# Optimization experiments

Measured on AMD Instinct MI355X. Metric: run time of the kernel, lower is better.

## Reference

```python
import jax, jax.numpy as jnp
import numpy as np

N = 50000   # nodes
E = 600000  # directed edges (self-loops added inside reference, per GCNConv default)
G = 64      # graphs in the batch
D = 128     # in_features
H = 128     # hidden_channels
C = 10      # num_classes


def setup_inputs() -> dict:
    key = jax.random.key(0)
    ks = jax.random.split(key, 9)
    x = jax.random.normal(ks[0], (N, D), dtype=jnp.float32)
    edge_index = jax.random.randint(ks[1], (2, E), 0, N, dtype=jnp.int64)
    batch = jnp.sort(jax.random.randint(ks[2], (N,), 0, G, dtype=jnp.int64))
    # GCNConv weights (glorot-ish scale) and biases; final linear layer
    W1 = jax.random.normal(ks[3], (D, H), dtype=jnp.float32) / np.sqrt(D).astype(np.float32)
    b1 = jnp.zeros((H,), dtype=jnp.float32)
    W2 = jax.random.normal(ks[4], (H, H), dtype=jnp.float32) / np.sqrt(H).astype(np.float32)
    b2 = jnp.zeros((H,), dtype=jnp.float32)
    Wlin = jax.random.normal(ks[5], (H, C), dtype=jnp.float32) / np.sqrt(H).astype(np.float32)
    blin = jnp.zeros((C,), dtype=jnp.float32)
    return {"x": x, "W1": W1, "b1": b1, "W2": W2, "b2": b2,
            "Wlin": Wlin, "blin": blin, "edge_index": edge_index, "batch": batch}


def _gcn_conv(x, W, b, row, col, norm):
    # x' = D^{-1/2}(A+I)D^{-1/2} (x W) + b ; aggregate messages from row (src) into col (dst)
    h = x @ W                                   # [N, H] dense GEMM
    msg = norm[:, None] * h[row]                # gather by source index [E+N, H]
    out = jax.ops.segment_sum(msg, col, num_segments=N)  # scatter-add to targets
    return out + b


def reference(x, W1, b1, W2, b2, Wlin, blin, edge_index, batch):
    loops = jnp.arange(N, dtype=edge_index.dtype)
    row = jnp.concatenate([edge_index[0], loops])   # sources (+ self loops)
    col = jnp.concatenate([edge_index[1], loops])   # targets (+ self loops)
    # symmetric degree normalization (degrees >= 1 thanks to self loops)
    deg = jax.ops.segment_sum(jnp.ones_like(col, dtype=jnp.float32), col, num_segments=N)
    dinv = jax.lax.rsqrt(deg)
    norm = dinv[row] * dinv[col]                    # [E+N]

    h = jax.nn.relu(_gcn_conv(x, W1, b1, row, col, norm))
    h = _gcn_conv(h, W2, b2, row, col, norm)

    # global mean pool over graphs
    sums = jax.ops.segment_sum(h, batch, num_segments=G)                       # [G, H]
    cnt = jax.ops.segment_sum(jnp.ones((N,), dtype=jnp.float32), batch, num_segments=G)
    pooled = sums / jnp.maximum(cnt, 1.0)[:, None]

    return pooled @ Wlin + blin                     # logits [G, C]
```

## Files before the change

### kernel.cpp

```cpp
#include <hip/hip_runtime.h>

#define NN 50000
#define NE 600000
#define NG 64
#define DIM 128
#define NCLS 10
#define SB 196
#define NNP 50176
#define KBLK 392
#define KCH 128
#define CAP 64
#define E2B ((NE / 2 + 255) / 256)
#define BSW_TAIL_START ((size_t)(NN >> 5) * 4096)

typedef unsigned short ushort;
typedef unsigned char uchar;
typedef __attribute__((ext_vector_type(8))) short short8;
typedef __attribute__((ext_vector_type(4))) float float4v;
typedef __attribute__((ext_vector_type(2))) float float2v;

__device__ __forceinline__ ushort f2bf(float f) {
    unsigned u = __float_as_uint(f);
    u += 0x7fff + ((u >> 16) & 1);
    return (ushort)(u >> 16);
}
__device__ __forceinline__ uchar f2fp8(float f) {
    int p = __builtin_amdgcn_cvt_pk_fp8_f32(f, f, 0, false);
    return (uchar)(p & 0xff);
}
__device__ __forceinline__ void accfp8(float* a, uint2 v) {
    float2v p0 = __builtin_amdgcn_cvt_pk_f32_fp8(v.x, false);
    float2v p1 = __builtin_amdgcn_cvt_pk_f32_fp8(v.x, true);
    float2v p2 = __builtin_amdgcn_cvt_pk_f32_fp8(v.y, false);
    float2v p3 = __builtin_amdgcn_cvt_pk_f32_fp8(v.y, true);
    a[0] += p0[0]; a[1] += p0[1]; a[2] += p1[0]; a[3] += p1[1];
    a[4] += p2[0]; a[5] += p2[1]; a[6] += p3[0]; a[7] += p3[1];
}
__device__ __forceinline__ uint2 ldrow(const uchar* __restrict__ Hs, int r, size_t off) {
    return *(const uint2*)(Hs + (size_t)r * DIM + off);
}

__global__ void k_init(int* __restrict__ cnt, const float* __restrict__ W1,
                       ushort* __restrict__ Wsw, float* __restrict__ T,
                       ushort* __restrict__ Bsw) {
    int b = blockIdx.x, t = threadIdx.x;
    if (b < SB) {
        int i = b * 256 + t;
        if (i < NN) cnt[i] = 0;
    } else if (b < SB + 64) {
        int tid = (b - SB) * 256 + t;
        int j = tid & 7;
        int lane = (tid >> 3) & 63;
        int frag = tid >> 9;
        int nt = frag >> 2, kc = frag & 3;
        int k = kc * 32 + (lane >> 4) * 8 + j;
        int n = nt * 16 + (lane & 15);
        Wsw[tid] = f2bf(W1[k * DIM + n]);
    } else if (b < SB + 64 + 784) {
        float4* w4 = (float4*)T;
        int base = (b - SB - 64) * 256 + t;
#pragma unroll
        for (int i = 0; i < 4; ++i)
            w4[base + i * 200704] = make_float4(0.f, 0.f, 0.f, 0.f);
    } else {
        int idx = (b - (SB + 64 + 784)) * 256 + t;
        ((float4*)(Bsw + BSW_TAIL_START))[idx] = make_float4(0.f, 0.f, 0.f, 0.f);
    }
}

__global__ void k_fill(const int* __restrict__ row, const int* __restrict__ col,
                       int* __restrict__ cnt, ushort* __restrict__ ell) {
    int e = (blockIdx.x * blockDim.x + threadIdx.x) * 2;
    if (e < NE) {
        int2 r = *(const int2*)(row + e);
        int2 c = *(const int2*)(col + e);
        int p0 = atomicAdd(&cnt[c.x], 1);
        if (p0 < CAP) ell[(size_t)c.x * CAP + p0] = (ushort)r.x;
        int p1 = atomicAdd(&cnt[c.y], 1);
        if (p1 < CAP) ell[(size_t)c.y * CAP + p1] = (ushort)r.y;
    }
}

__global__ __launch_bounds__(256) void k_gemm_mfma(const float* __restrict__ Ain,
                                                   const ushort* __restrict__ Wsw,
                                                   const int* __restrict__ cnt,
                                                   uchar* __restrict__ Hs) {
    const int t = threadIdx.x;
    const int wave = t >> 6, lane = t & 63;
    const int m = lane & 15, quad = lane >> 4;
    const int row0 = blockIdx.x * 64 + wave * 16;

    short8 bfrag[8][4];
#pragma unroll
    for (int nt = 0; nt < 8; ++nt)
#pragma unroll
        for (int kc = 0; kc < 4; ++kc)
            bfrag[nt][kc] = *(const short8*)(Wsw + ((nt * 4 + kc) * 64 + lane) * 8);

    float4v acc[8];
#pragma unroll
    for (int nt = 0; nt < 8; ++nt) acc[nt] = (float4v){0.f, 0.f, 0.f, 0.f};

    const int row = row0 + m;
    const int rclamp = row < NN ? row : NN - 1;

#pragma unroll
    for (int kc = 0; kc < 4; ++kc) {
        const float* ap = Ain + (size_t)rclamp * DIM + kc * 32 + quad * 8;
        float4 v0 = *(const float4*)ap;
        float4 v1 = *(const float4*)(ap + 4);
        union { short8 v; ushort u[8]; } tmp;
        tmp.u[0] = f2bf(v0.x); tmp.u[1] = f2bf(v0.y);
        tmp.u[2] = f2bf(v0.z); tmp.u[3] = f2bf(v0.w);
        tmp.u[4] = f2bf(v1.x); tmp.u[5] = f2bf(v1.y);
        tmp.u[6] = f2bf(v1.z); tmp.u[7] = f2bf(v1.w);
        short8 a = tmp.v;
#pragma unroll
        for (int nt = 0; nt < 8; ++nt)
            acc[nt] = __builtin_amdgcn_mfma_f32_16x16x32_bf16(a, bfrag[nt][kc], acc[nt], 0, 0, 0);
    }

#pragma unroll
    for (int reg = 0; reg < 4; ++reg) {
        int r = row0 + quad * 4 + reg;
        if (r < NN) {
            float d = rsqrtf(1.0f + (float)cnt[r]);
#pragma unroll
            for (int nt = 0; nt < 8; ++nt)
                Hs[(size_t)r * DIM + nt * 16 + m] = f2fp8(d * acc[nt][reg]);
        }
    }
}

__global__ __launch_bounds__(256) void k_gather_ell(const ushort* __restrict__ ell,
                                                    const int* __restrict__ deg,
                                                    const int* __restrict__ batch,
                                                    const float* __restrict__ bias,
                                                    const uchar* __restrict__ Hs,
                                                    float* __restrict__ T,
                                                    ushort* __restrict__ Bsw) {
    const int t = threadIdx.x, b = blockIdx.x;
    const int tn = t >> 4, lane = t & 15;
    const int node = b * 16 + tn;
    const ushort* rowp = ell + (size_t)node * CAP;
    int end = min(deg[node], CAP);
    const float d = rsqrtf(1.0f + (float)deg[node]);
    float* Trow = T + (size_t)batch[node] * NNP;
    const size_t off = (size_t)lane * 8;

    float a[8] = {0.f, 0.f, 0.f, 0.f, 0.f, 0.f, 0.f, 0.f};
    accfp8(a, ldrow(Hs, node, off));
    if (lane == 0) atomicAdd(&Trow[node], d);

    int e = 0;
    for (; e + 8 <= end; e += 8) {
        uint4 iv = *(const uint4*)(rowp + e);
        int r0 = iv.x & 0xffff, r1 = iv.x >> 16;
        int r2 = iv.y & 0xffff, r3 = iv.y >> 16;
        int r4 = iv.z & 0xffff, r5 = iv.z >> 16;
        int r6 = iv.w & 0xffff, r7 = iv.w >> 16;
        if (lane < 8) atomicAdd(&Trow[rowp[e + lane]], d);
        uint2 v0 = ldrow(Hs, r0, off), v1 = ldrow(Hs, r1, off);
        uint2 v2 = ldrow(Hs, r2, off), v3 = ldrow(Hs, r3, off);
        uint2 v4 = ldrow(Hs, r4, off), v5 = ldrow(Hs, r5, off);
        uint2 v6 = ldrow(Hs, r6, off), v7 = ldrow(Hs, r7, off);
        accfp8(a, v0); accfp8(a, v1); accfp8(a, v2); accfp8(a, v3);
        accfp8(a, v4); accfp8(a, v5); accfp8(a, v6); accfp8(a, v7);
    }
    for (; e + 4 <= end; e += 4) {
        uint2 lv = *(const uint2*)(rowp + e);
        int r0 = lv.x & 0xffff, r1 = lv.x >> 16;
        int r2 = lv.y & 0xffff, r3 = lv.y >> 16;
        if (lane < 4) atomicAdd(&Trow[rowp[e + lane]], d);
        uint2 v0 = ldrow(Hs, r0, off), v1 = ldrow(Hs, r1, off);
        uint2 v2 = ldrow(Hs, r2, off), v3 = ldrow(Hs, r3, off);
        accfp8(a, v0); accfp8(a, v1); accfp8(a, v2); accfp8(a, v3);
    }
    for (; e < end; ++e) {
        int r = rowp[e];
        if (lane == 0) atomicAdd(&Trow[r], d);
        accfp8(a, ldrow(Hs, r, off));
    }

    float4 b0 = *(const float4*)(bias + off);
    float4 b1 = *(const float4*)(bias + off + 4);
    a[0] = fmaxf(fmaf(a[0], d, b0.x), 0.f); a[1] = fmaxf(fmaf(a[1], d, b0.y), 0.f);
    a[2] = fmaxf(fmaf(a[2], d, b0.z), 0.f); a[3] = fmaxf(fmaf(a[3], d, b0.w), 0.f);
    a[4] = fmaxf(fmaf(a[4], d, b1.x), 0.f); a[5] = fmaxf(fmaf(a[5], d, b1.y), 0.f);
    a[6] = fmaxf(fmaf(a[6], d, b1.z), 0.f); a[7] = fmaxf(fmaf(a[7], d, b1.w), 0.f);

    __shared__ ushort Lb[16][128];
    union { short8 v; ushort u[8]; } st;
    st.u[0] = f2bf(d * a[0]); st.u[1] = f2bf(d * a[1]);
    st.u[2] = f2bf(d * a[2]); st.u[3] = f2bf(d * a[3]);
    st.u[4] = f2bf(d * a[4]); st.u[5] = f2bf(d * a[5]);
    st.u[6] = f2bf(d * a[6]); st.u[7] = f2bf(d * a[7]);
    *(short8*)(&Lb[tn][lane * 8]) = st.v;
    __syncthreads();

    const int nt = t >> 5, idx = t & 31;
    const int a_rel = (idx >> 4) & 1, fb = (idx >> 3) & 1, f7 = idx & 7;
    const int feat = nt * 16 + fb * 8 + f7;
    const int nl = a_rel * 8;
    uint4 o;
    o.x = (unsigned)Lb[nl + 0][feat] | ((unsigned)Lb[nl + 1][feat] << 16);
    o.y = (unsigned)Lb[nl + 2][feat] | ((unsigned)Lb[nl + 3][feat] << 16);
    o.z = (unsigned)Lb[nl + 4][feat] | ((unsigned)Lb[nl + 5][feat] << 16);
    o.w = (unsigned)Lb[nl + 6][feat] | ((unsigned)Lb[nl + 7][feat] << 16);
    size_t base = (size_t)(b >> 1) * 4096 + (size_t)nt * 512
                + (size_t)((b & 1) * 2 + a_rel) * 128 + (size_t)fb * 64 + (size_t)f7 * 8;
    *(uint4*)(Bsw + base) = o;
}

__global__ __launch_bounds__(256) void k_pool_gemm(const float* __restrict__ T,
                                                   const ushort* __restrict__ Bsw,
                                                   float* __restrict__ partial) {
    const int t = threadIdx.x;
    const int wave = t >> 6, lane = t & 63;
    const int m = lane & 15, quad = lane >> 4;
    const int g = wave * 16 + m;
    const int k0 = blockIdx.x * KCH;

    float4v acc[8];
#pragma unroll
    for (int nt = 0; nt < 8; ++nt) acc[nt] = (float4v){0.f, 0.f, 0.f, 0.f};

#pragma unroll
    for (int s = 0; s < KCH / 32; ++s) {
        const int kb = k0 + s * 32 + quad * 8;
        const float* ap = T + (size_t)g * NNP + kb;
        float4 a0 = *(const float4*)ap;
        float4 a1 = *(const float4*)(ap + 4);
        union { short8 v; ushort u[8]; } af;
        af.u[0] = f2bf(a0.x); af.u[1] = f2bf(a0.y);
        af.u[2] = f2bf(a0.z); af.u[3] = f2bf(a0.w);
        af.u[4] = f2bf(a1.x); af.u[5] = f2bf(a1.y);
        af.u[6] = f2bf(a1.z); af.u[7] = f2bf(a1.w);

        const int t32 = (k0 >> 5) + s;
        const ushort* bb = Bsw + (size_t)t32 * 4096 + (size_t)lane * 8;
#pragma unroll
        for (int nt = 0; nt < 8; ++nt) {
            short8 bv = *(const short8*)(bb + nt * 512);
            acc[nt] = __builtin_amdgcn_mfma_f32_16x16x32_bf16(af.v, bv, acc[nt], 0, 0, 0);
        }
    }

    float* dst = partial + (size_t)blockIdx.x * (NG * DIM);
#pragma unroll
    for (int reg = 0; reg < 4; ++reg) {
        int gg = wave * 16 + quad * 4 + reg;
#pragma unroll
        for (int nt = 0; nt < 8; ++nt)
            dst[gg * DIM + nt * 16 + m] = acc[nt][reg];
    }
}

__global__ __launch_bounds__(512) void k_final(const float* __restrict__ partial,
                                               const float* __restrict__ W2,
                                               const float* __restrict__ b2,
                                               const float* __restrict__ Wlin,
                                               const float* __restrict__ blin,
                                               const int* __restrict__ batch,
                                               float* __restrict__ out) {
    const int g = blockIdx.x;
    const int t = threadIdx.x;
    const int c = t & 127, h = t >> 7;

    float s0 = 0.f, s1 = 0.f;
    const float* pp = partial + (size_t)h * 98 * (NG * DIM) + g * DIM + c;
#pragma unroll 7
    for (int i = 0; i < 98; i += 2) {
        s0 += pp[(size_t)i * (NG * DIM)];
        s1 += pp[(size_t)(i + 1) * (NG * DIM)];
    }

    __shared__ float red[512];
    __shared__ float Pl[DIM];
    __shared__ float pooled[DIM];
    red[t] = s0 + s1;
    __syncthreads();
    if (t < 128) Pl[t] = red[t] + red[t + 128] + red[t + 256] + red[t + 384];
    __syncthreads();
    if (t < 128) {
        float acc = 0.f;
        for (int k = 0; k < DIM; ++k) acc += Pl[k] * W2[k * DIM + t];
        int start;
        { int a = 0, bb = NN; while (a < bb) { int mm = (a + bb) >> 1; if (batch[mm] < g) a = mm + 1; else bb = mm; } start = a; }
        int endp;
        { int a = 0, bb = NN; while (a < bb) { int mm = (a + bb) >> 1; if (batch[mm] < g + 1) a = mm + 1; else bb = mm; } endp = a; }
        const int cnt = endp - start;
        pooled[t] = (cnt > 0) ? (acc / (float)cnt + b2[t]) : 0.f;
    }
    __syncthreads();
    if (t < NCLS) {
        float s2 = blin[t];
        for (int k = 0; k < DIM; ++k) s2 += pooled[k] * Wlin[k * NCLS + t];
        out[g * NCLS + t] = s2;
    }
}

extern "C" void kernel_launch(void* const* d_in, const int* in_sizes, int n_in,
                              void* d_out, int out_size, void* d_ws, size_t ws_size,
                              hipStream_t stream) {
    const float* x    = (const float*)d_in[0];
    const float* W1   = (const float*)d_in[1];
    const float* b1   = (const float*)d_in[2];
    const float* W2   = (const float*)d_in[3];
    const float* b2   = (const float*)d_in[4];
    const float* Wlin = (const float*)d_in[5];
    const float* blin = (const float*)d_in[6];
    const int* eidx   = (const int*)d_in[7];
    const int* batch  = (const int*)d_in[8];
    float* out = (float*)d_out;

    char* ws = (char*)d_ws;
    int*    cnt   = (int*)(ws + 0);
    ushort* Wsw   = (ushort*)(ws + 400704);
    ushort* ell   = (ushort*)(ws + 433472);
    uchar*  Hs1   = (uchar*)(ws + 6833472);
    float*  T     = (float*)(ws + 13233472);
    ushort* Bsw   = (ushort*)(ws + 26078528);
    float*  partial=(float*)(ws + 38923584);

    const int* erow = eidx;
    const int* ecol = eidx + NE;

    k_init<<<SB + 64 + 784 + 12, 256, 0, stream>>>(cnt, W1, Wsw, T, Bsw);
    k_fill<<<E2B, 256, 0, stream>>>(erow, ecol, cnt, ell);

    const int gemm_grid = (NN + 63) / 64;
    const int node_grid = NN / 16;

    k_gemm_mfma<<<gemm_grid, 256, 0, stream>>>(x, Wsw, cnt, Hs1);
    k_gather_ell<<<node_grid, 256, 0, stream>>>(ell, cnt, batch, b1, Hs1, T, Bsw);

    k_pool_gemm<<<KBLK, 256, 0, stream>>>(T, Bsw, partial);

    k_final<<<NG, 512, 0, stream>>>(partial, W2, b2, Wlin, blin, batch, out);
}
```

Baseline: 201.2 us.

## Parallelize partial reduction, widen edge fill, and lower GEMM register pressure

Moves the cross-block pooled-sum reduction out of the 64-block final kernel into a separate wide kernel that accumulates into a zeroed buffer with atomics. The final kernel then only does the small matvecs. The edge-fill kernel handles four edges per thread with vector loads and issues its atomics together. The feature GEMM loads weight fragments per K chunk instead of holding all of them in registers, targeting higher occupancy. In exchange it adds a launch and float atomics, which make the summation order nondeterministic.

```diff
diff --git a/kernel.cpp b/kernel.cpp
--- a/kernel.cpp
+++ b/kernel.cpp
@@ -10,7 +10,7 @@
 #define KBLK 392
 #define KCH 128
 #define CAP 64
-#define E2B ((NE / 2 + 255) / 256)
+#define E4B ((NE / 4 + 255) / 256)
 #define BSW_TAIL_START ((size_t)(NN >> 5) * 4096)
 
 typedef unsigned short ushort;
@@ -42,7 +42,7 @@
 
 __global__ void k_init(int* __restrict__ cnt, const float* __restrict__ W1,
                        ushort* __restrict__ Wsw, float* __restrict__ T,
-                       ushort* __restrict__ Bsw) {
+                       ushort* __restrict__ Bsw, float* __restrict__ P) {
     int b = blockIdx.x, t = threadIdx.x;
     if (b < SB) {
         int i = b * 256 + t;
@@ -62,62 +62,76 @@
 #pragma unroll
         for (int i = 0; i < 4; ++i)
             w4[base + i * 200704] = make_float4(0.f, 0.f, 0.f, 0.f);
-    } else {
+    } else if (b < SB + 64 + 784 + 12) {
         int idx = (b - (SB + 64 + 784)) * 256 + t;
         ((float4*)(Bsw + BSW_TAIL_START))[idx] = make_float4(0.f, 0.f, 0.f, 0.f);
+    } else {
+#pragma unroll
+        for (int i = 0; i < 8; ++i)
+            ((float4*)P)[i * 256 + t] = make_float4(0.f, 0.f, 0.f, 0.f);
     }
 }
 
 __global__ void k_fill(const int* __restrict__ row, const int* __restrict__ col,
                        int* __restrict__ cnt, ushort* __restrict__ ell) {
-    int e = (blockIdx.x * blockDim.x + threadIdx.x) * 2;
+    int e = (blockIdx.x * blockDim.x + threadIdx.x) * 4;
     if (e < NE) {
-        int2 r = *(const int2*)(row + e);
-        int2 c = *(const int2*)(col + e);
+        int4 r = *(const int4*)(row + e);
+        int4 c = *(const int4*)(col + e);
         int p0 = atomicAdd(&cnt[c.x], 1);
+        int p1 = atomicAdd(&cnt[c.y], 1);
+        int p2 = atomicAdd(&cnt[c.z], 1);
+        int p3 = atomicAdd(&cnt[c.w], 1);
         if (p0 < CAP) ell[(size_t)c.x * CAP + p0] = (ushort)r.x;
-        int p1 = atomicAdd(&cnt[c.y], 1);
         if (p1 < CAP) ell[(size_t)c.y * CAP + p1] = (ushort)r.y;
-    }
-}
-
-__global__ __launch_bounds__(256) void k_gemm_mfma(const float* __restrict__ Ain,
-                                                   const ushort* __restrict__ Wsw,
-                                                   const int* __restrict__ cnt,
-                                                   uchar* __restrict__ Hs) {
+        if (p2 < CAP) ell[(size_t)c.z * CAP + p2] = (ushort)r.z;
+        if (p3 < CAP) ell[(size_t)c.w * CAP + p3] = (ushort)r.w;
+    }
+}
+
+__global__ __launch_bounds__(256, 4) void k_gemm_mfma(const float* __restrict__ Ain,
+                                                      const ushort* __restrict__ Wsw,
+                                                      const int* __restrict__ cnt,
+                                                      uchar* __restrict__ Hs) {
     const int t = threadIdx.x;
     const int wave = t >> 6, lane = t & 63;
     const int m = lane & 15, quad = lane >> 4;
     const int row0 = blockIdx.x * 64 + wave * 16;
-
-    short8 bfrag[8][4];
-#pragma unroll
-    for (int nt = 0; nt < 8; ++nt)
-#pragma unroll
-        for (int kc = 0; kc < 4; ++kc)
-            bfrag[nt][kc] = *(const short8*)(Wsw + ((nt * 4 + kc) * 64 + lane) * 8);
-
-    float4v acc[8];
-#pragma unroll
-    for (int nt = 0; nt < 8; ++nt) acc[nt] = (float4v){0.f, 0.f, 0.f, 0.f};
-
     const int row = row0 + m;
     const int rclamp = row < NN ? row : NN - 1;
 
+    float4 v[8];
+    const float* ap = Ain + (size_t)rclamp * DIM + quad * 8;
 #pragma unroll
     for (int kc = 0; kc < 4; ++kc) {
-        const float* ap = Ain + (size_t)rclamp * DIM + kc * 32 + quad * 8;
-        float4 v0 = *(const float4*)ap;
-        float4 v1 = *(const float4*)(ap + 4);
-        union { short8 v; ushort u[8]; } tmp;
-        tmp.u[0] = f2bf(v0.x); tmp.u[1] = f2bf(v0.y);
-        tmp.u[2] = f2bf(v0.z); tmp.u[3] = f2bf(v0.w);
-        tmp.u[4] = f2bf(v1.x); tmp.u[5] = f2bf(v1.y);
-        tmp.u[6] = f2bf(v1.z); tmp.u[7] = f2bf(v1.w);
-        short8 a = tmp.v;
+        v[2 * kc]     = *(const float4*)(ap + kc * 32);
+        v[2 * kc + 1] = *(const float4*)(ap + kc * 32 + 4);
+    }
+    short8 afrag[4];
+#pragma unroll
+    for (int kc = 0; kc < 4; ++kc) {
+        union { short8 s; ushort u[8]; } tmp;
+        tmp.u[0] = f2bf(v[2 * kc].x);     tmp.u[1] = f2bf(v[2 * kc].y);
+        tmp.u[2] = f2bf(v[2 * kc].z);     tmp.u[3] = f2bf(v[2 * kc].w);
+        tmp.u[4] = f2bf(v[2 * kc + 1].x); tmp.u[5] = f2bf(v[2 * kc + 1].y);
+        tmp.u[6] = f2bf(v[2 * kc + 1].z); tmp.u[7] = f2bf(v[2 * kc + 1].w);
+        afrag[kc] = tmp.s;
+    }
+
+    float4v acc[8];
+#pragma unroll
+    for (int nt = 0; nt < 8; ++nt) acc[nt] = (float4v){0.f, 0.f, 0.f, 0.f};
+
+#pragma unroll
+    for (int kc = 0; kc < 4; ++kc) {
+        const ushort* wp = Wsw + (size_t)kc * 512 + (size_t)lane * 8;
+        short8 bfr[8];
 #pragma unroll
         for (int nt = 0; nt < 8; ++nt)
-            acc[nt] = __builtin_amdgcn_mfma_f32_16x16x32_bf16(a, bfrag[nt][kc], acc[nt], 0, 0, 0);
+            bfr[nt] = *(const short8*)(wp + (size_t)nt * 2048);
+#pragma unroll
+        for (int nt = 0; nt < 8; ++nt)
+            acc[nt] = __builtin_amdgcn_mfma_f32_16x16x32_bf16(afrag[kc], bfr[nt], acc[nt], 0, 0, 0);
     }
 
 #pragma unroll
@@ -256,7 +270,18 @@
     }
 }
 
-__global__ __launch_bounds__(512) void k_final(const float* __restrict__ partial,
+__global__ __launch_bounds__(256) void k_red(const float* __restrict__ partial,
+                                             float* __restrict__ P) {
+    int tid = blockIdx.x * 256 + threadIdx.x;
+    int elem = tid & 8191, h = tid >> 13;
+    const float* pp = partial + (size_t)h * 49 * (NG * DIM) + elem;
+    float s = 0.f;
+#pragma unroll
+    for (int i = 0; i < 49; ++i) s += pp[(size_t)i * (NG * DIM)];
+    atomicAdd(&P[elem], s);
+}
+
+__global__ __launch_bounds__(128) void k_final(const float* __restrict__ P,
                                                const float* __restrict__ W2,
                                                const float* __restrict__ b2,
                                                const float* __restrict__ Wlin,
@@ -265,33 +290,19 @@
                                                float* __restrict__ out) {
     const int g = blockIdx.x;
     const int t = threadIdx.x;
-    const int c = t & 127, h = t >> 7;
-
-    float s0 = 0.f, s1 = 0.f;
-    const float* pp = partial + (size_t)h * 98 * (NG * DIM) + g * DIM + c;
-#pragma unroll 7
-    for (int i = 0; i < 98; i += 2) {
-        s0 += pp[(size_t)i * (NG * DIM)];
-        s1 += pp[(size_t)(i + 1) * (NG * DIM)];
-    }
-
-    __shared__ float red[512];
+    int start;
+    { int a = 0, bb = NN; while (a < bb) { int mm = (a + bb) >> 1; if (batch[mm] < g) a = mm + 1; else bb = mm; } start = a; }
+    int endp;
+    { int a = 0, bb = NN; while (a < bb) { int mm = (a + bb) >> 1; if (batch[mm] < g + 1) a = mm + 1; else bb = mm; } endp = a; }
+    const int cnt = endp - start;
+
     __shared__ float Pl[DIM];
     __shared__ float pooled[DIM];
-    red[t] = s0 + s1;
+    Pl[t] = P[g * DIM + t];
     __syncthreads();
-    if (t < 128) Pl[t] = red[t] + red[t + 128] + red[t + 256] + red[t + 384];
-    __syncthreads();
-    if (t < 128) {
-        float acc = 0.f;
-        for (int k = 0; k < DIM; ++k) acc += Pl[k] * W2[k * DIM + t];
-        int start;
-        { int a = 0, bb = NN; while (a < bb) { int mm = (a + bb) >> 1; if (batch[mm] < g) a = mm + 1; else bb = mm; } start = a; }
-        int endp;
-        { int a = 0, bb = NN; while (a < bb) { int mm = (a + bb) >> 1; if (batch[mm] < g + 1) a = mm + 1; else bb = mm; } endp = a; }
-        const int cnt = endp - start;
-        pooled[t] = (cnt > 0) ? (acc / (float)cnt + b2[t]) : 0.f;
-    }
+    float acc = 0.f;
+    for (int k = 0; k < DIM; ++k) acc += Pl[k] * W2[k * DIM + t];
+    pooled[t] = (cnt > 0) ? (acc / (float)cnt + b2[t]) : 0.f;
     __syncthreads();
     if (t < NCLS) {
         float s2 = blin[t];
@@ -322,12 +333,13 @@
     float*  T     = (float*)(ws + 13233472);
     ushort* Bsw   = (ushort*)(ws + 26078528);
     float*  partial=(float*)(ws + 38923584);
+    float*  P     = (float*)(ws + 51768640);
 
     const int* erow = eidx;
     const int* ecol = eidx + NE;
 
-    k_init<<<SB + 64 + 784 + 12, 256, 0, stream>>>(cnt, W1, Wsw, T, Bsw);
-    k_fill<<<E2B, 256, 0, stream>>>(erow, ecol, cnt, ell);
+    k_init<<<SB + 64 + 784 + 12 + 1, 256, 0, stream>>>(cnt, W1, Wsw, T, Bsw, P);
+    k_fill<<<E4B, 256, 0, stream>>>(erow, ecol, cnt, ell);
 
     const int gemm_grid = (NN + 63) / 64;
     const int node_grid = NN / 16;
@@ -336,6 +348,7 @@
     k_gather_ell<<<node_grid, 256, 0, stream>>>(ell, cnt, batch, b1, Hs1, T, Bsw);
 
     k_pool_gemm<<<KBLK, 256, 0, stream>>>(T, Bsw, partial);
-
-    k_final<<<NG, 512, 0, stream>>>(partial, W2, b2, Wlin, blin, batch, out);
-}
+    k_red<<<256, 256, 0, stream>>>(partial, P);
+
+    k_final<<<NG, 128, 0, stream>>>(P, W2, b2, Wlin, blin, batch, out);
+}
```

New measurement: 193.2 us. -3.9%, faster.
